# Kernel optimization log

Hardware: AMD Instinct MI355X
Metric: run time of the kernel (lower is better)

The kernel has to match this reference:

```python
import jax, jax.numpy as jnp
import numpy as np

N_HEADS = 4
T_OUT = 24  # total T; y has T - t_in steps


def setup_inputs() -> dict:
    key = jax.random.key(0)
    k1, k2, k3, k4 = jax.random.split(key, 4)
    B, t_in, N, C, K = 2, 12, 10000, 16, 17  # K = k + 1 (self)
    x = jax.random.normal(k1, (B, t_in, N, C), dtype=jnp.float32)
    nearest_nodes = jax.random.randint(k2, (N, K), 0, N, dtype=jnp.int32)
    nearest_dists = jax.random.uniform(k3, (N, K), dtype=jnp.float32)
    shrink_w = jax.random.normal(k4, (T_OUT - t_in, t_in * N_HEADS), dtype=jnp.float32) * 0.1
    shrink_b = jnp.zeros((T_OUT - t_in,), dtype=jnp.float32)
    return {"x": x, "nearest_nodes": nearest_nodes, "nearest_dists": nearest_dists,
            "shrink_w": shrink_w, "shrink_b": shrink_b}


def reference(x, nearest_nodes, nearest_dists, shrink_w, shrink_b):
    B, t_in, N, C = x.shape
    H = N_HEADS
    # sigma = nearest_dists.max() / sigma_ratio, with sigma_ratio = 1
    sigma = jnp.max(nearest_dists)
    lam = jnp.arange(1, H + 1, dtype=x.dtype) / H  # (H,)
    # distance weights per head: (N, K, H)
    w = jnp.exp(-(nearest_dists[..., None] ** 2) * lam / (sigma ** 2))
    w = jnp.where((nearest_nodes == -1)[..., None], 0.0, w)
    w = jnp.where(w < 1e-8, 0.0, w)
    # pad node at index N; -1 neighbors map to pad (weight already zero)
    pad_x = jnp.concatenate([x, jnp.zeros_like(x[:, :, :1])], axis=2)  # (B,T,N+1,C)
    idx = jnp.where(nearest_nodes == -1, N, nearest_nodes)  # (N, K)
    g = pad_x[:, :, idx]  # (B, t_in, N, K, C) neighbor gather
    # weighted reduce over neighbor axis -> (B, t_in, N, H, C)
    agg = jnp.einsum('btnkc,nkh->btnhc', g, w)
    # (B, N, C, t_in*H)
    a = jnp.transpose(agg, (0, 2, 4, 1, 3)).reshape(B, N, C, t_in * H)
    y = a @ shrink_w.T + shrink_b  # (B, N, C, T - t_in)
    y = jnp.transpose(y, (0, 3, 1, 2))  # (B, T - t_in, N, C)
    y = jax.nn.selu(y)  # CustomActivationFunction default mode='selu'
    return jnp.concatenate([x, y], axis=1)  # (B, T, N, C)
```

## Files before the change

kernel.cpp:

```cpp
#include <hip/hip_runtime.h>
#include <hip/hip_bf16.h>
#include <math.h>

#define NB      2
#define T_IN    12
#define T_OUT_  24
#define O_OUT   12
#define NN      10000
#define CC      16
#define KK      17
#define HH      4
#define JJ      48
#define PL      24
#define XCHN    40
#define CHN     250
#define XBLK    (PL * XCHN)
#define SBLK    167
#define GW      4
#define GBLK    (NN / GW)
#define PSTR    68
#define ANS     (PL * PSTR)

typedef float v2f __attribute__((ext_vector_type(2)));

__device__ __forceinline__ unsigned int f2bf(float f) {
    union { float f; unsigned int u; } v; v.f = f;
    unsigned int r = v.u + 0x7FFFu + ((v.u >> 16) & 1u);
    return r >> 16;
}
__device__ __forceinline__ float bf_lo(unsigned int u) {
    union { unsigned int u; float f; } v; v.u = u << 16; return v.f;
}
__device__ __forceinline__ float bf_hi(unsigned int u) {
    union { unsigned int u; float f; } v; v.u = u & 0xffff0000u; return v.f;
}
__device__ __forceinline__ v2f bfpair(unsigned int u) {
    v2f r;
    r.x = bf_lo(u);
    r.y = bf_hi(u);
    return r;
}

__device__ __forceinline__ void wave_fence() {
#if __has_builtin(__builtin_amdgcn_wave_barrier)
    __builtin_amdgcn_wave_barrier();
#else
    __syncthreads();
#endif
}

__global__ __launch_bounds__(256) void setup_kernel(
    const float* __restrict__ x,
    const float* __restrict__ dists, int ndists,
    float* __restrict__ out,
    unsigned short* __restrict__ xt,
    int* __restrict__ sigma_bits)
{
    const int tid = threadIdx.x;
    if (blockIdx.x < XBLK) {
        const int p  = blockIdx.x / XCHN;
        const int ch = blockIdx.x % XCHN;
        const int b = p / T_IN, t = p % T_IN;
        const int n0 = ch * CHN;
        const float* xp = x + (long)(p * NN + n0) * CC;
        float* op = out + (long)((b * T_OUT_ + t) * NN + n0) * CC;
        uint2* xtp = (uint2*)xt + (long)n0 * (PL * 4) + p * 4;
        for (int i = tid; i < CHN * 4; i += 256) {
            const int nl = i >> 2, q = i & 3;
            const float4 v = *(const float4*)(xp + i * 4);
            *(float4*)(op + i * 4) = v;
            uint2 pk;
            pk.x = f2bf(v.x) | (f2bf(v.y) << 16);
            pk.y = f2bf(v.z) | (f2bf(v.w) << 16);
            xtp[(long)nl * (PL * 4) + q] = pk;
        }
    } else {
        const int sb = blockIdx.x - XBLK;
        float m = 0.0f;
        const int nv4 = ndists >> 2;
        const float4* d4 = (const float4*)dists;
        for (int i = sb * 256 + tid; i < nv4; i += SBLK * 256) {
            float4 v = d4[i];
            m = fmaxf(fmaxf(m, fmaxf(v.x, v.y)), fmaxf(v.z, v.w));
        }
        for (int i = (nv4 << 2) + sb * 256 + tid; i < ndists; i += SBLK * 256)
            m = fmaxf(m, dists[i]);
        #pragma unroll
        for (int off = 32; off > 0; off >>= 1)
            m = fmaxf(m, __shfl_down(m, off, 64));
        __shared__ float sm[4];
        int lane = tid & 63, wid = tid >> 6;
        if (lane == 0) sm[wid] = m;
        __syncthreads();
        if (tid == 0) {
            float mm = fmaxf(fmaxf(sm[0], sm[1]), fmaxf(sm[2], sm[3]));
            atomicMax(sigma_bits, __float_as_int(mm));
        }
    }
}

__global__ __launch_bounds__(256) void fused_kernel(
    const unsigned short* __restrict__ xt,
    const int*   __restrict__ nodes,
    const float* __restrict__ dists,
    const int*   __restrict__ sigma_bits,
    const float* __restrict__ Wm,
    const float* __restrict__ bias,
    float* __restrict__ out)
{
    const int tid  = threadIdx.x;
    const int wave = tid >> 6;
    const int lane = tid & 63;
    const int n0   = blockIdx.x * GW;

    __shared__ float    W_s[O_OUT * JJ];
    __shared__ float    b_s[O_OUT];
    __shared__ unsigned lidx[GW * KK];
    __shared__ uint2    lw2[GW * KK];
    __shared__ float    a_s[GW * ANS];

    for (int i = tid; i < O_OUT * JJ; i += 256) W_s[i] = Wm[i];
    if (tid < O_OUT) b_s[tid] = bias[tid];
    if (tid < GW * KK) {
        const float sigma  = __int_as_float(*sigma_bits);
        const float inv_s2 = 1.0f / (sigma * sigma);
        const int   nd = nodes[n0 * KK + tid];
        const float dd = dists[n0 * KK + tid];
        const float e1 = expf(-dd * dd * inv_s2 * 0.25f);
        float w0 = e1, w1 = e1 * e1, w2 = w1 * e1, w3 = w1 * w1;
        if (nd == -1) { w0 = w1 = w2 = w3 = 0.f; }
        if (w0 < 1e-8f) w0 = 0.f;
        if (w1 < 1e-8f) w1 = 0.f;
        if (w2 < 1e-8f) w2 = 0.f;
        if (w3 < 1e-8f) w3 = 0.f;
        lidx[tid] = (unsigned)(((nd < 0) ? 0 : nd) * (PL * CC * 2));
        lw2[tid]  = make_uint2(f2bf(w0) | (f2bf(w1) << 16),
                               f2bf(w2) | (f2bf(w3) << 16));
    }
    __syncthreads();

    const int rb = wave * KK;
    float* abase = a_s + wave * ANS;
    if (lane < 48) {
        const char* xtb = (const char*)xt;
        uint4 gv[KK];
        #pragma unroll
        for (int k = 0; k < KK; ++k)
            gv[k] = *(const uint4*)(xtb + lidx[rb + k] + (lane << 4));

        v2f acc[HH][4];
        #pragma unroll
        for (int h = 0; h < HH; ++h)
            #pragma unroll
            for (int p = 0; p < 4; ++p) acc[h][p] = (v2f){0.f, 0.f};

        #pragma unroll
        for (int k = 0; k < KK; ++k) {
            const uint2 wp = lw2[rb + k];
            const v2f vw0 = {bf_lo(wp.x), bf_lo(wp.x)};
            const v2f vw1 = {bf_hi(wp.x), bf_hi(wp.x)};
            const v2f vw2 = {bf_lo(wp.y), bf_lo(wp.y)};
            const v2f vw3 = {bf_hi(wp.y), bf_hi(wp.y)};
            v2f g[4];
            g[0] = bfpair(gv[k].x);
            g[1] = bfpair(gv[k].y);
            g[2] = bfpair(gv[k].z);
            g[3] = bfpair(gv[k].w);
            #pragma unroll
            for (int p = 0; p < 4; ++p) {
                acc[0][p] += g[p] * vw0;
                acc[1][p] += g[p] * vw1;
                acc[2][p] += g[p] * vw2;
                acc[3][p] += g[p] * vw3;
            }
        }

        const int plane = lane >> 1;
        const int oct   = lane & 1;
        float* ap = abase + plane * PSTR + oct * 32;
        #pragma unroll
        for (int j = 0; j < 8; ++j) {
            const int p = j >> 1, e = j & 1;
            *(float4*)(ap + j * 4) = make_float4(acc[0][p][e], acc[1][p][e],
                                                 acc[2][p][e], acc[3][p][e]);
        }
    }
    wave_fence();

    const float kScale = 1.0507009873554805f;
    const float kAlpha = 1.6732632423543772f;
    const int n = n0 + wave;
    const int c = lane & 15;
    const int d = lane >> 4;
    float y[3][NB];
    #pragma unroll
    for (int i = 0; i < 3; ++i) {
        const float bv = b_s[d * 3 + i];
        y[i][0] = bv; y[i][1] = bv;
    }
    #pragma unroll
    for (int t = 0; t < T_IN; ++t) {
        const float4 a0 = *(const float4*)(abase + t * PSTR + c * 4);
        const float4 a1 = *(const float4*)(abase + (T_IN + t) * PSTR + c * 4);
        #pragma unroll
        for (int i = 0; i < 3; ++i) {
            const float4 wv = *(const float4*)(W_s + (d * 3 + i) * JJ + t * 4);
            y[i][0] += a0.x * wv.x + a0.y * wv.y + a0.z * wv.z + a0.w * wv.w;
            y[i][1] += a1.x * wv.x + a1.y * wv.y + a1.z * wv.z + a1.w * wv.w;
        }
    }
    #pragma unroll
    for (int i = 0; i < 3; ++i)
        #pragma unroll
        for (int b = 0; b < NB; ++b) {
            float v = y[i][b];
            v = (v > 0.0f) ? kScale * v : kScale * kAlpha * (__expf(v) - 1.0f);
            const int o = d * 3 + i;
            out[((long)(b * T_OUT_ + T_IN + o) * NN + n) * CC + c] = v;
        }
}

extern "C" void kernel_launch(void* const* d_in, const int* in_sizes, int n_in,
                              void* d_out, int out_size, void* d_ws, size_t ws_size,
                              hipStream_t stream) {
    const float* x     = (const float*)d_in[0];
    const int*   nodes = (const int*)  d_in[1];
    const float* dists = (const float*)d_in[2];
    const float* Wm    = (const float*)d_in[3];
    const float* bias  = (const float*)d_in[4];
    float* out = (float*)d_out;

    char* ws = (char*)d_ws;
    int*            sigma_bits = (int*)ws;
    unsigned short* xt         = (unsigned short*)(ws + 1024);

    const int ndists = in_sizes[2];
    setup_kernel<<<XBLK + SBLK, 256, 0, stream>>>(x, dists, ndists, out, xt,
                                                  sigma_bits);
    fused_kernel<<<GBLK, 256, 0, stream>>>(xt, nodes, dists, sigma_bits,
                                           Wm, bias, out);
}
```

Baseline: 111.8 us.

## Retile transpose, pre-transpose shrink weights, drop LDS weight staging, restructure projection

The setup kernel now tiles the x transpose over 16-node chunks across all 24 planes, and it adds one block that writes a transposed copy of shrink_w plus the bias into workspace. The fused kernel no longer stages W and bias in shared memory; it reads the transposed weights straight from global (cache) memory. Per-neighbor weights are kept as fp32 float4 instead of packed bf16, and gathers are issued inside the k loop rather than prefetched into 17 registers. The projection splits the time axis across lane groups, with each lane computing all 12 outputs and then combining them by cross-lane shuffles. The aim is to cut LDS traffic, register pressure and the per-block weight loads, at the cost of less memory-level parallelism in the gather loop and extra shuffle work.

```diff
diff --git a/kernel.cpp b/kernel.cpp
--- a/kernel.cpp
+++ b/kernel.cpp
@@ -12,9 +12,8 @@
 #define HH      4
 #define JJ      48
 #define PL      24
-#define XCHN    40
-#define CHN     250
-#define XBLK    (PL * XCHN)
+#define TN      16
+#define XBLK    (NN / TN)
 #define SBLK    167
 #define GW      4
 #define GBLK    (NN / GW)
@@ -35,10 +34,7 @@
     union { unsigned int u; float f; } v; v.u = u & 0xffff0000u; return v.f;
 }
 __device__ __forceinline__ v2f bfpair(unsigned int u) {
-    v2f r;
-    r.x = bf_lo(u);
-    r.y = bf_hi(u);
-    return r;
+    v2f r; r.x = bf_lo(u); r.y = bf_hi(u); return r;
 }
 
 __device__ __forceinline__ void wave_fence() {
@@ -52,29 +48,28 @@
 __global__ __launch_bounds__(256) void setup_kernel(
     const float* __restrict__ x,
     const float* __restrict__ dists, int ndists,
+    const float* __restrict__ Wm,
+    const float* __restrict__ bias,
     float* __restrict__ out,
     unsigned short* __restrict__ xt,
+    float* __restrict__ wt,
     int* __restrict__ sigma_bits)
 {
     const int tid = threadIdx.x;
     if (blockIdx.x < XBLK) {
-        const int p  = blockIdx.x / XCHN;
-        const int ch = blockIdx.x % XCHN;
-        const int b = p / T_IN, t = p % T_IN;
-        const int n0 = ch * CHN;
-        const float* xp = x + (long)(p * NN + n0) * CC;
-        float* op = out + (long)((b * T_OUT_ + t) * NN + n0) * CC;
-        uint2* xtp = (uint2*)xt + (long)n0 * (PL * 4) + p * 4;
-        for (int i = tid; i < CHN * 4; i += 256) {
-            const int nl = i >> 2, q = i & 3;
-            const float4 v = *(const float4*)(xp + i * 4);
-            *(float4*)(op + i * 4) = v;
+        const int n0 = blockIdx.x * TN;
+        for (int i = tid; i < PL * TN * 4; i += 256) {
+            const int p = i >> 6, rem = i & 63, nl = rem >> 2, q = rem & 3;
+            const float4 v =
+                *(const float4*)(x + ((long)p * NN + n0 + nl) * CC + q * 4);
+            const int b = p / T_IN, t = p % T_IN;
+            *(float4*)(out + ((long)(b * T_OUT_ + t) * NN + n0 + nl) * CC + q * 4) = v;
             uint2 pk;
             pk.x = f2bf(v.x) | (f2bf(v.y) << 16);
             pk.y = f2bf(v.z) | (f2bf(v.w) << 16);
-            xtp[(long)nl * (PL * 4) + q] = pk;
-        }
-    } else {
+            ((uint2*)xt)[(long)(n0 + nl) * (PL * 4) + p * 4 + q] = pk;
+        }
+    } else if (blockIdx.x < XBLK + SBLK) {
         const int sb = blockIdx.x - XBLK;
         float m = 0.0f;
         const int nv4 = ndists >> 2;
@@ -96,6 +91,10 @@
             float mm = fmaxf(fmaxf(sm[0], sm[1]), fmaxf(sm[2], sm[3]));
             atomicMax(sigma_bits, __float_as_int(mm));
         }
+    } else {
+        for (int i = tid; i < O_OUT * JJ; i += 256)
+            wt[i] = Wm[(i % O_OUT) * JJ + (i / O_OUT)];
+        if (tid < O_OUT) wt[O_OUT * JJ + tid] = bias[tid];
     }
 }
 
@@ -104,8 +103,7 @@
     const int*   __restrict__ nodes,
     const float* __restrict__ dists,
     const int*   __restrict__ sigma_bits,
-    const float* __restrict__ Wm,
-    const float* __restrict__ bias,
+    const float* __restrict__ wt,
     float* __restrict__ out)
 {
     const int tid  = threadIdx.x;
@@ -113,14 +111,10 @@
     const int lane = tid & 63;
     const int n0   = blockIdx.x * GW;
 
-    __shared__ float    W_s[O_OUT * JJ];
-    __shared__ float    b_s[O_OUT];
     __shared__ unsigned lidx[GW * KK];
-    __shared__ uint2    lw2[GW * KK];
+    __shared__ float4   lwf[GW * KK];
     __shared__ float    a_s[GW * ANS];
 
-    for (int i = tid; i < O_OUT * JJ; i += 256) W_s[i] = Wm[i];
-    if (tid < O_OUT) b_s[tid] = bias[tid];
     if (tid < GW * KK) {
         const float sigma  = __int_as_float(*sigma_bits);
         const float inv_s2 = 1.0f / (sigma * sigma);
@@ -134,8 +128,7 @@
         if (w2 < 1e-8f) w2 = 0.f;
         if (w3 < 1e-8f) w3 = 0.f;
         lidx[tid] = (unsigned)(((nd < 0) ? 0 : nd) * (PL * CC * 2));
-        lw2[tid]  = make_uint2(f2bf(w0) | (f2bf(w1) << 16),
-                               f2bf(w2) | (f2bf(w3) << 16));
+        lwf[tid]  = make_float4(w0, w1, w2, w3);
     }
     __syncthreads();
 
@@ -143,11 +136,6 @@
     float* abase = a_s + wave * ANS;
     if (lane < 48) {
         const char* xtb = (const char*)xt;
-        uint4 gv[KK];
-        #pragma unroll
-        for (int k = 0; k < KK; ++k)
-            gv[k] = *(const uint4*)(xtb + lidx[rb + k] + (lane << 4));
-
         v2f acc[HH][4];
         #pragma unroll
         for (int h = 0; h < HH; ++h)
@@ -156,22 +144,18 @@
 
         #pragma unroll
         for (int k = 0; k < KK; ++k) {
-            const uint2 wp = lw2[rb + k];
-            const v2f vw0 = {bf_lo(wp.x), bf_lo(wp.x)};
-            const v2f vw1 = {bf_hi(wp.x), bf_hi(wp.x)};
-            const v2f vw2 = {bf_lo(wp.y), bf_lo(wp.y)};
-            const v2f vw3 = {bf_hi(wp.y), bf_hi(wp.y)};
+            const unsigned off = lidx[rb + k];
+            const uint4  gv = *(const uint4*)(xtb + off + (lane << 4));
+            const float4 wv = lwf[rb + k];
             v2f g[4];
-            g[0] = bfpair(gv[k].x);
-            g[1] = bfpair(gv[k].y);
-            g[2] = bfpair(gv[k].z);
-            g[3] = bfpair(gv[k].w);
+            g[0] = bfpair(gv.x); g[1] = bfpair(gv.y);
+            g[2] = bfpair(gv.z); g[3] = bfpair(gv.w);
             #pragma unroll
             for (int p = 0; p < 4; ++p) {
-                acc[0][p] += g[p] * vw0;
-                acc[1][p] += g[p] * vw1;
-                acc[2][p] += g[p] * vw2;
-                acc[3][p] += g[p] * vw3;
+                acc[0][p] += g[p] * wv.x;
+                acc[1][p] += g[p] * wv.y;
+                acc[2][p] += g[p] * wv.z;
+                acc[3][p] += g[p] * wv.w;
             }
         }
 
@@ -187,37 +171,50 @@
     }
     wave_fence();
 
+    const int n = n0 + wave;
+    const int c = lane & 15;
+    const int r = lane >> 4;
+    v2f y[O_OUT];
+    #pragma unroll
+    for (int o = 0; o < O_OUT; ++o) y[o] = (v2f){0.f, 0.f};
+
+    #pragma unroll
+    for (int tt = 0; tt < 3; ++tt) {
+        const int t = r * 3 + tt;
+        const float4 a0 = *(const float4*)(abase + t * PSTR + c * 4);
+        const float4 a1 = *(const float4*)(abase + (T_IN + t) * PSTR + c * 4);
+        const float* wr = wt + t * JJ;
+        #pragma unroll
+        for (int h = 0; h < HH; ++h) {
+            const v2f av = {((const float*)&a0)[h], ((const float*)&a1)[h]};
+            #pragma unroll
+            for (int o = 0; o < O_OUT; ++o)
+                y[o] += av * wr[h * O_OUT + o];
+        }
+    }
+
+    #pragma unroll
+    for (int o = 0; o < O_OUT; ++o) {
+        y[o].x += __shfl_xor(y[o].x, 16, 64);
+        y[o].y += __shfl_xor(y[o].y, 16, 64);
+        y[o].x += __shfl_xor(y[o].x, 32, 64);
+        y[o].y += __shfl_xor(y[o].y, 32, 64);
+    }
+
     const float kScale = 1.0507009873554805f;
     const float kAlpha = 1.6732632423543772f;
-    const int n = n0 + wave;
-    const int c = lane & 15;
-    const int d = lane >> 4;
-    float y[3][NB];
+    const float* bias_t = wt + O_OUT * JJ;
     #pragma unroll
     for (int i = 0; i < 3; ++i) {
-        const float bv = b_s[d * 3 + i];
-        y[i][0] = bv; y[i][1] = bv;
-    }
-    #pragma unroll
-    for (int t = 0; t < T_IN; ++t) {
-        const float4 a0 = *(const float4*)(abase + t * PSTR + c * 4);
-        const float4 a1 = *(const float4*)(abase + (T_IN + t) * PSTR + c * 4);
-        #pragma unroll
-        for (int i = 0; i < 3; ++i) {
-            const float4 wv = *(const float4*)(W_s + (d * 3 + i) * JJ + t * 4);
-            y[i][0] += a0.x * wv.x + a0.y * wv.y + a0.z * wv.z + a0.w * wv.w;
-            y[i][1] += a1.x * wv.x + a1.y * wv.y + a1.z * wv.z + a1.w * wv.w;
-        }
-    }
-    #pragma unroll
-    for (int i = 0; i < 3; ++i)
+        const int o = r * 3 + i;
+        const float bv = bias_t[o];
         #pragma unroll
         for (int b = 0; b < NB; ++b) {
-            float v = y[i][b];
+            float v = ((b == 0) ? y[o].x : y[o].y) + bv;
             v = (v > 0.0f) ? kScale * v : kScale * kAlpha * (__expf(v) - 1.0f);
-            const int o = d * 3 + i;
             out[((long)(b * T_OUT_ + T_IN + o) * NN + n) * CC + c] = v;
         }
+    }
 }
 
 extern "C" void kernel_launch(void* const* d_in, const int* in_sizes, int n_in,
@@ -232,11 +229,12 @@
 
     char* ws = (char*)d_ws;
     int*            sigma_bits = (int*)ws;
-    unsigned short* xt         = (unsigned short*)(ws + 1024);
+    float*          wt         = (float*)(ws + 64);
+    unsigned short* xt         = (unsigned short*)(ws + 4096);
 
     const int ndists = in_sizes[2];
-    setup_kernel<<<XBLK + SBLK, 256, 0, stream>>>(x, dists, ndists, out, xt,
-                                                  sigma_bits);
+    setup_kernel<<<XBLK + SBLK + 1, 256, 0, stream>>>(
+        x, dists, ndists, Wm, bias, out, xt, wt, sigma_bits);
     fused_kernel<<<GBLK, 256, 0, stream>>>(xt, nodes, dists, sigma_bits,
-                                           Wm, bias, out);
-}
+                                           wt, out);
+}
```

After: 113.9 us. No clear change (+1.9%).
